# Kernel tuning notes

Hardware: AMD Instinct MI355X
Metric: run time of the kernel (lower is better)

## Reference

```python
import jax, jax.numpy as jnp
import numpy as np

T = 2048      # tokens (flattened batch*seq)
HID = 2048    # hidden_size
H = 16        # num heads
D = HID // H  # head_dim = 128
EPS = 1e-5
THETA = 1000000.0


def setup_inputs() -> dict:
    key = jax.random.key(0)
    k0, k1, k2 = jax.random.split(key, 3)
    return {
        "hidden_states": jax.random.normal(k0, (T, HID), jnp.float32),
        "positions": jnp.arange(T, dtype=jnp.int32),
        "w_qkv": jax.random.normal(k1, (HID, 3 * HID), jnp.float32) * 0.02,
        "q_norm_w": jnp.ones((HID,), jnp.float32),
        "k_norm_w": jnp.ones((HID,), jnp.float32),
        "w_o": jax.random.normal(k2, (HID, HID), jnp.float32) * 0.02,
    }


def _rmsnorm(x, w):
    # RMSNorm over the full flat q/k vector (q_size / kv_size), as in forward_native
    var = jnp.mean(jnp.square(x.astype(jnp.float32)), axis=-1, keepdims=True)
    return (x.astype(jnp.float32) * jax.lax.rsqrt(var + EPS)).astype(x.dtype) * w


def _rope(x, positions):
    # NEOX-style rotary over full head_dim. x: [T, H, D]
    half = D // 2
    inv_freq = 1.0 / (THETA ** (jnp.arange(half, dtype=jnp.float32) / half))
    ang = positions.astype(jnp.float32)[:, None] * inv_freq  # [T, half]
    cos = jnp.cos(ang)[:, None, :]  # [T, 1, half]
    sin = jnp.sin(ang)[:, None, :]
    x1, x2 = x[..., :half], x[..., half:]
    return jnp.concatenate([x1 * cos - x2 * sin, x2 * cos + x1 * sin], axis=-1)


def reference(hidden_states, positions, w_qkv, q_norm_w, k_norm_w, w_o):
    qkv = hidden_states @ w_qkv                      # [T, 3*HID]
    q, k, v = jnp.split(qkv, [HID, 2 * HID], axis=-1)
    q = _rmsnorm(q, q_norm_w)
    k = _rmsnorm(k, k_norm_w)
    q = _rope(q.reshape(T, H, D), positions)
    k = _rope(k.reshape(T, H, D), positions)
    v = v.reshape(T, H, D)
    scale = D ** -0.5
    scores = jnp.einsum('qhd,khd->hqk', q, k) * scale   # [H, T, T]
    causal = jnp.tril(jnp.ones((T, T), bool))
    scores = jnp.where(causal[None], scores, jnp.finfo(scores.dtype).min)
    probs = jax.nn.softmax(scores, axis=-1)
    attn = jnp.einsum('hqk,khd->qhd', probs, v).reshape(T, HID)
    return attn @ w_o
```

## Files before the change

kernel.cpp:

```cpp
#include <hip/hip_runtime.h>
#include <hip/hip_bf16.h>

typedef __attribute__((ext_vector_type(8))) short bf16x8;
typedef __attribute__((ext_vector_type(4))) float f32x4;

__device__ inline unsigned short f2b(float x) {
  __hip_bfloat16 b = __float2bfloat16(x);
  return *reinterpret_cast<unsigned short*>(&b);
}
__device__ inline float b2f(unsigned short u) {
  return __bfloat162float(*reinterpret_cast<const __hip_bfloat16*>(&u));
}

#define GAS(p) ((const __attribute__((address_space(1))) void*)(p))
#define LAS(p) ((__attribute__((address_space(3))) void*)(p))

__global__ __launch_bounds__(256) void cast_f32_bf16(const float* __restrict__ X,
                                                     unsigned short* __restrict__ Y, int n4) {
  int i = blockIdx.x * 256 + threadIdx.x;
  if (i < n4) {
    float4 v = reinterpret_cast<const float4*>(X)[i];
    ushort4 o;
    o.x = f2b(v.x); o.y = f2b(v.y); o.z = f2b(v.z); o.w = f2b(v.w);
    reinterpret_cast<ushort4*>(Y)[i] = o;
  }
}

__global__ __launch_bounds__(256) void tcast(const float* __restrict__ W,
                                             unsigned short* __restrict__ Wt, int K, int N) {
  __shared__ float tile[32][33];
  int n0 = blockIdx.x * 32, k0 = blockIdx.y * 32;
  int tx = threadIdx.x & 31, ty = threadIdx.x >> 5;
#pragma unroll
  for (int i = 0; i < 32; i += 8)
    tile[ty + i][tx] = W[(size_t)(k0 + ty + i) * N + n0 + tx];
  __syncthreads();
#pragma unroll
  for (int i = 0; i < 32; i += 8)
    Wt[(size_t)(n0 + ty + i) * K + k0 + tx] = f2b(tile[tx][ty + i]);
}

__global__ __launch_bounds__(256) void vtrans(const float* __restrict__ qkv,
                                              unsigned short* __restrict__ Vt) {
  __shared__ unsigned short tile[32][33];
  int c0 = blockIdx.x * 32;
  int t0 = blockIdx.y * 32;
  int tx = threadIdx.x & 31, ty = threadIdx.x >> 5;
#pragma unroll
  for (int i = 0; i < 32; i += 8)
    tile[ty + i][tx] = f2b(qkv[(size_t)(t0 + ty + i) * 6144 + 4096 + c0 + tx]);
  __syncthreads();
#pragma unroll
  for (int i = 0; i < 32; i += 8)
    Vt[(size_t)(c0 + ty + i) * 2048 + t0 + tx] = tile[tx][ty + i];
}

__global__ __launch_bounds__(256) void gemm_bt(const unsigned short* __restrict__ A,
                                               const unsigned short* __restrict__ Bt,
                                               float* __restrict__ C, int M, int N, int K) {
  __shared__ unsigned short As[128 * 32];
  __shared__ unsigned short Bs[128 * 32];
  const int tid = threadIdx.x;
  const int w = tid >> 6, l = tid & 63;
  const int lr = l & 15, lg = l >> 4;
  const int wm = (w >> 1) << 6, wn = (w & 1) << 6;
  const size_t bm = (size_t)blockIdx.y * 128, bn = (size_t)blockIdx.x * 128;

  const int srow = tid >> 2;
  const int scol = (tid & 3) << 3;
  const unsigned short* Ag = A + (bm + srow) * (size_t)K + scol;
  const unsigned short* Bg = Bt + (bn + srow) * (size_t)K + scol;
  unsigned short* Al = As + w * 512;
  unsigned short* Bl = Bs + w * 512;

  f32x4 acc[4][4] = {};

  for (int k0 = 0; k0 < K; k0 += 32) {
    __syncthreads();
    __builtin_amdgcn_global_load_lds(GAS(Ag + k0), LAS(Al), 16, 0, 0);
    __builtin_amdgcn_global_load_lds(GAS(Ag + (size_t)64 * K + k0), LAS(Al + 2048), 16, 0, 0);
    __builtin_amdgcn_global_load_lds(GAS(Bg + k0), LAS(Bl), 16, 0, 0);
    __builtin_amdgcn_global_load_lds(GAS(Bg + (size_t)64 * K + k0), LAS(Bl + 2048), 16, 0, 0);
    __syncthreads();

    bf16x8 af[4], bfr[4];
#pragma unroll
    for (int mi = 0; mi < 4; ++mi)
      af[mi] = *reinterpret_cast<const bf16x8*>(&As[(wm + mi * 16 + lr) * 32 + lg * 8]);
#pragma unroll
    for (int ni = 0; ni < 4; ++ni)
      bfr[ni] = *reinterpret_cast<const bf16x8*>(&Bs[(wn + ni * 16 + lr) * 32 + lg * 8]);
#pragma unroll
    for (int mi = 0; mi < 4; ++mi)
#pragma unroll
      for (int ni = 0; ni < 4; ++ni)
        acc[mi][ni] = __builtin_amdgcn_mfma_f32_16x16x32_bf16(af[mi], bfr[ni], acc[mi][ni], 0, 0, 0);
  }

#pragma unroll
  for (int mi = 0; mi < 4; ++mi)
#pragma unroll
    for (int ni = 0; ni < 4; ++ni)
#pragma unroll
      for (int r = 0; r < 4; ++r) {
        size_t row = bm + wm + mi * 16 + lg * 4 + r;
        size_t col = bn + wn + ni * 16 + lr;
        C[row * N + col] = acc[mi][ni][r];
      }
}

__global__ __launch_bounds__(256) void rms_rope(const float* __restrict__ qkv,
                                                const int* __restrict__ pos,
                                                const float* __restrict__ qw,
                                                const float* __restrict__ kw,
                                                unsigned short* __restrict__ qb,
                                                unsigned short* __restrict__ kb) {
  const int t = blockIdx.x;
  const float* row = qkv + (size_t)t * 6144;
  __shared__ float redq[4], redk[4];
  __shared__ float cs[64], sn[64];
  const int tid = threadIdx.x, w = tid >> 6, l = tid & 63;

  float sq = 0.f, sk = 0.f;
#pragma unroll
  for (int i = 0; i < 8; ++i) {
    float a = row[tid + i * 256]; sq += a * a;
    float b = row[2048 + tid + i * 256]; sk += b * b;
  }
#pragma unroll
  for (int m = 32; m >= 1; m >>= 1) { sq += __shfl_xor(sq, m, 64); sk += __shfl_xor(sk, m, 64); }
  if (l == 0) { redq[w] = sq; redk[w] = sk; }
  if (tid < 64) {
    float fr = exp2f(-(float)tid * 0.31143075889569016f);
    float ang = (float)pos[t] * fr;
    cs[tid] = cosf(ang);
    sn[tid] = sinf(ang);
  }
  __syncthreads();
  float rq = rsqrtf((redq[0] + redq[1] + redq[2] + redq[3]) * (1.f / 2048.f) + 1e-5f);
  float rk = rsqrtf((redk[0] + redk[1] + redk[2] + redk[3]) * (1.f / 2048.f) + 1e-5f);
  const float rqs = rq * 0.12753102543609887f;

  unsigned short* qo = qb + (size_t)t * 2048;
  unsigned short* ko = kb + (size_t)t * 2048;
#pragma unroll
  for (int pp = 0; pp < 4; ++pp) {
    int pr = tid + pp * 256;
    int h = pr >> 6, j = pr & 63;
    int b0 = h * 128 + j;
    float c = cs[j], s = sn[j];
    float x1 = row[b0] * rqs * qw[b0];
    float x2 = row[b0 + 64] * rqs * qw[b0 + 64];
    qo[b0]      = f2b(x1 * c - x2 * s);
    qo[b0 + 64] = f2b(x2 * c + x1 * s);
    float y1 = row[2048 + b0] * rk * kw[b0];
    float y2 = row[2048 + b0 + 64] * rk * kw[b0 + 64];
    ko[b0]      = f2b(y1 * c - y2 * s);
    ko[b0 + 64] = f2b(y2 * c + y1 * s);
  }
}

__device__ __forceinline__ void stage_kv(const unsigned short* __restrict__ kb_h,
                                         const unsigned short* __restrict__ vt_h,
                                         int k0, int w, int l,
                                         unsigned short* Ks, unsigned short* Vs) {
  const int r0 = l >> 4, cph = l & 15;
#pragma unroll
  for (int rb = 0; rb < 16; rb += 4) {
    int row = w * 16 + rb + r0;
    int clog = (cph & 8) | ((cph & 7) ^ (row & 7));
    const unsigned short* src = kb_h + (size_t)(k0 + row) * 2048 + clog * 8;
    __builtin_amdgcn_global_load_lds(GAS(src), LAS((char*)Ks + (w * 16 + rb) * 256), 16, 0, 0);
  }
  const int r0v = l >> 3, cpv = l & 7;
#pragma unroll
  for (int rb = 0; rb < 32; rb += 8) {
    int row = w * 32 + rb + r0v;
    int clog = cpv ^ (row & 7);
    const unsigned short* src = vt_h + (size_t)row * 2048 + k0 + clog * 8;
    __builtin_amdgcn_global_load_lds(GAS(src), LAS((char*)Vs + (w * 32 + rb) * 128), 16, 0, 0);
  }
}

template <bool MASKED>
__device__ __forceinline__ void attn_tile(int k0, int qrbase, int lr, int lg,
                                          const bf16x8 (&qf)[4],
                                          const unsigned short* __restrict__ Ks,
                                          const unsigned short* __restrict__ Vs,
                                          unsigned short* __restrict__ PsW,
                                          f32x4 (&oacc)[8], float (&mrow)[4], float (&lrow)[4]) {
  f32x4 s[4] = {};
  __builtin_amdgcn_s_setprio(1);
#pragma unroll
  for (int kc = 0; kc < 4; ++kc)
#pragma unroll
    for (int cg = 0; cg < 4; ++cg) {
      int key = cg * 16 + lr;
      int c = 4 * kc + lg;
      int cswz = (c & 8) | ((c & 7) ^ (key & 7));
      bf16x8 kf = *reinterpret_cast<const bf16x8*>(&Ks[key * 128 + cswz * 8]);
      s[cg] = __builtin_amdgcn_mfma_f32_16x16x32_bf16(qf[kc], kf, s[cg], 0, 0, 0);
    }
  __builtin_amdgcn_s_setprio(0);

#pragma unroll
  for (int r = 0; r < 4; ++r) {
    const int qr = qrbase + lg * 4 + r;
    float p0 = s[0][r], p1 = s[1][r], p2 = s[2][r], p3 = s[3][r];
    if (MASKED) {
      if (k0 + lr > qr)      p0 = -1e30f;
      if (k0 + 16 + lr > qr) p1 = -1e30f;
      if (k0 + 32 + lr > qr) p2 = -1e30f;
      if (k0 + 48 + lr > qr) p3 = -1e30f;
    }
    float mx = fmaxf(fmaxf(p0, p1), fmaxf(p2, p3));
#pragma unroll
    for (int m = 8; m >= 1; m >>= 1) mx = fmaxf(mx, __shfl_xor(mx, m, 16));
    float mnew = fmaxf(mrow[r], mx);
    float corr = exp2f(mrow[r] - mnew);
    p0 = exp2f(p0 - mnew); p1 = exp2f(p1 - mnew);
    p2 = exp2f(p2 - mnew); p3 = exp2f(p3 - mnew);
    lrow[r] = lrow[r] * corr + ((p0 + p1) + (p2 + p3));
    mrow[r] = mnew;
#pragma unroll
    for (int ni = 0; ni < 8; ++ni) oacc[ni][r] *= corr;
    const int prow = (lg * 4 + r) * 72;
    PsW[prow + lr]      = f2b(p0);
    PsW[prow + 16 + lr] = f2b(p1);
    PsW[prow + 32 + lr] = f2b(p2);
    PsW[prow + 48 + lr] = f2b(p3);
  }

  __builtin_amdgcn_s_setprio(1);
#pragma unroll
  for (int ks = 0; ks < 2; ++ks) {
    bf16x8 pf = *reinterpret_cast<const bf16x8*>(&PsW[lr * 72 + ks * 32 + lg * 8]);
#pragma unroll
    for (int ni = 0; ni < 8; ++ni) {
      int d = ni * 16 + lr;
      int c = ks * 4 + lg;
      int cswz = c ^ (d & 7);
      bf16x8 vf = *reinterpret_cast<const bf16x8*>(&Vs[d * 64 + cswz * 8]);
      oacc[ni] = __builtin_amdgcn_mfma_f32_16x16x32_bf16(pf, vf, oacc[ni], 0, 0, 0);
    }
  }
  __builtin_amdgcn_s_setprio(0);
}

__global__ __launch_bounds__(256) void attn_part(const unsigned short* __restrict__ qb,
                                                 const unsigned short* __restrict__ kb,
                                                 const unsigned short* __restrict__ vt,
                                                 unsigned short* __restrict__ Op,
                                                 float* __restrict__ ml) {
  __shared__ unsigned short Ks[64 * 128];
  __shared__ unsigned short Vs[128 * 64];
  __shared__ unsigned short Ps[4][16 * 72];
  const int qt = blockIdx.x, h = blockIdx.y, sp = blockIdx.z;
  const int q0 = qt * 64;
  const int kbeg = sp * 256;
  if (kbeg >= q0 + 64) return;
  const int tid = threadIdx.x, w = tid >> 6, l = tid & 63;
  const int lr = l & 15, lg = l >> 4;
  const int qrbase = q0 + w * 16;

  bf16x8 qf[4];
  {
    const unsigned short* qp = qb + (size_t)(qrbase + lr) * 2048 + h * 128;
#pragma unroll
    for (int kc = 0; kc < 4; ++kc)
      qf[kc] = *reinterpret_cast<const bf16x8*>(qp + kc * 32 + lg * 8);
  }
  f32x4 oacc[8] = {};
  float mrow[4], lrow[4];
#pragma unroll
  for (int r = 0; r < 4; ++r) { mrow[r] = -1e30f; lrow[r] = 0.f; }

  const unsigned short* kb_h = kb + h * 128;
  const unsigned short* vt_h = vt + (size_t)h * 128 * 2048;

  const int kstop_full = min(kbeg + 256, q0);
  for (int k0 = kbeg; k0 < kstop_full; k0 += 64) {
    __syncthreads();
    stage_kv(kb_h, vt_h, k0, w, l, Ks, Vs);
    __syncthreads();
    attn_tile<false>(k0, qrbase, lr, lg, qf, Ks, Vs, Ps[w], oacc, mrow, lrow);
  }
  if (q0 >= kbeg && q0 < kbeg + 256) {
    __syncthreads();
    stage_kv(kb_h, vt_h, q0, w, l, Ks, Vs);
    __syncthreads();
    attn_tile<true>(q0, qrbase, lr, lg, qf, Ks, Vs, Ps[w], oacc, mrow, lrow);
  }

#pragma unroll
  for (int r = 0; r < 4; ++r)
#pragma unroll
    for (int m = 8; m >= 1; m >>= 1) lrow[r] += __shfl_xor(lrow[r], m, 16);

  const int g = qt >> 2, j = qt & 3;
  const size_t u = (size_t)h * 144 + (g + 1) * (2 * g + j) + sp;
  const size_t baserow = u * 64 + w * 16;
#pragma unroll
  for (int ni = 0; ni < 8; ++ni)
#pragma unroll
    for (int r = 0; r < 4; ++r)
      Op[(baserow + lg * 4 + r) * 128 + ni * 16 + lr] = f2b(oacc[ni][r]);
  if (lr == 0) {
#pragma unroll
    for (int r = 0; r < 4; ++r) {
      size_t mi = (baserow + lg * 4 + r) * 2;
      ml[mi] = mrow[r]; ml[mi + 1] = lrow[r];
    }
  }
}

__global__ __launch_bounds__(256) void attn_combine(const unsigned short* __restrict__ Op,
                                                    const float* __restrict__ ml,
                                                    unsigned short* __restrict__ ob) {
  const int qt = blockIdx.x, h = blockIdx.y;
  const int q0 = qt * 64;
  const int g = qt >> 2, j = qt & 3;
  const int ns = g + 1;
  const size_t ubase = (size_t)h * 144 + (g + 1) * (2 * g + j);
  const int t = threadIdx.x;
  const int row = t >> 2, dp = (t & 3) * 32;

  float m_s[8], l_s[8];
  float M = -1e30f;
#pragma unroll
  for (int s = 0; s < 8; ++s) {
    if (s < ns) {
      size_t mi = ((ubase + s) * 64 + row) * 2;
      m_s[s] = ml[mi]; l_s[s] = ml[mi + 1];
    } else { m_s[s] = -1e30f; l_s[s] = 0.f; }
    M = fmaxf(M, m_s[s]);
  }
  float L = 0.f, wgt[8];
#pragma unroll
  for (int s = 0; s < 8; ++s) { wgt[s] = exp2f(m_s[s] - M); L += l_s[s] * wgt[s]; }
  float invL = 1.f / L;

  float acc[32];
#pragma unroll
  for (int jj = 0; jj < 32; ++jj) acc[jj] = 0.f;
#pragma unroll
  for (int s = 0; s < 8; ++s) {
    if (s < ns) {
      const unsigned short* op = Op + ((ubase + s) * 64 + row) * 128 + dp;
      float wg = wgt[s] * invL;
#pragma unroll
      for (int jj = 0; jj < 32; jj += 8) {
        bf16x8 v = *reinterpret_cast<const bf16x8*>(op + jj);
#pragma unroll
        for (int e = 0; e < 8; ++e) acc[jj + e] += wg * b2f((unsigned short)v[e]);
      }
    }
  }
  unsigned short* o = ob + (size_t)(q0 + row) * 2048 + h * 128 + dp;
#pragma unroll
  for (int jj = 0; jj < 32; ++jj) o[jj] = f2b(acc[jj]);
}

extern "C" void kernel_launch(void* const* d_in, const int* in_sizes, int n_in,
                              void* d_out, int out_size, void* d_ws, size_t ws_size,
                              hipStream_t stream) {
  const float* hs   = (const float*)d_in[0];
  const int*   pos  = (const int*)d_in[1];
  const float* wqkv = (const float*)d_in[2];
  const float* qnw  = (const float*)d_in[3];
  const float* knw  = (const float*)d_in[4];
  const float* wo   = (const float*)d_in[5];
  float* out = (float*)d_out;

  char* ws = (char*)d_ws;
  size_t off = 0;
  auto take = [&](size_t bytes) {
    char* p = ws + off;
    off = (off + bytes + 255) & ~(size_t)255;
    return p;
  };
  unsigned short* hidA  = (unsigned short*)take(2048ull * 2048 * 2);
  unsigned short* wqkvT = (unsigned short*)take(6144ull * 2048 * 2);
  unsigned short* woT   = (unsigned short*)take(2048ull * 2048 * 2);
  float*          qkvF  = (float*)take(2048ull * 6144 * 4);
  unsigned short* qbv   = (unsigned short*)take(2048ull * 2048 * 2);
  unsigned short* kbv   = (unsigned short*)take(2048ull * 2048 * 2);
  unsigned short* vtb   = (unsigned short*)take(2048ull * 2048 * 2);
  unsigned short* attnb = (unsigned short*)take(2048ull * 2048 * 2);
  unsigned short* Opart = (unsigned short*)qkvF;
  float*          mlb   = (float*)((char*)qkvF + 40ull * 1024 * 1024);

  cast_f32_bf16<<<4096, 256, 0, stream>>>(hs, hidA, 1048576);
  tcast<<<dim3(192, 64), 256, 0, stream>>>(wqkv, wqkvT, 2048, 6144);
  tcast<<<dim3(64, 64), 256, 0, stream>>>(wo, woT, 2048, 2048);
  gemm_bt<<<dim3(48, 16), 256, 0, stream>>>(hidA, wqkvT, qkvF, 2048, 6144, 2048);
  rms_rope<<<2048, 256, 0, stream>>>(qkvF, pos, qnw, knw, qbv, kbv);
  vtrans<<<dim3(64, 64), 256, 0, stream>>>(qkvF, vtb);
  attn_part<<<dim3(32, 16, 8), 256, 0, stream>>>(qbv, kbv, vtb, Opart, mlb);
  attn_combine<<<dim3(32, 16), 256, 0, stream>>>(Opart, mlb, attnb);
  gemm_bt<<<dim3(16, 16), 256, 0, stream>>>(attnb, woT, out, 2048, 2048, 2048);
}
```

Baseline: 374.7 us.

## Double-buffer K/V tiles in attention and widen split-K chunks to 512

The attention partial kernel now keeps two K/V shared-memory buffers. It prefetches the next 64-key tile while computing the current one, which cuts the synchronisations per tile from two to one. The key split grows from 256 to 512 keys, so there are at most four partials per query tile and the combine kernel reads fewer of them. The partial buffer now uses a simple dense [split, head, qtile] indexing. Costs are double the LDS per block, which may lower occupancy, and fewer blocks in the grid for parallelism.

```diff
diff --git a/kernel.cpp b/kernel.cpp
--- a/kernel.cpp
+++ b/kernel.cpp
@@ -252,17 +252,24 @@
                                                  const unsigned short* __restrict__ vt,
                                                  unsigned short* __restrict__ Op,
                                                  float* __restrict__ ml) {
-  __shared__ unsigned short Ks[64 * 128];
-  __shared__ unsigned short Vs[128 * 64];
+  __shared__ unsigned short Ks[2][64 * 128];
+  __shared__ unsigned short Vs[2][128 * 64];
   __shared__ unsigned short Ps[4][16 * 72];
   const int qt = blockIdx.x, h = blockIdx.y, sp = blockIdx.z;
   const int q0 = qt * 64;
-  const int kbeg = sp * 256;
+  const int kbeg = sp * 512;
   if (kbeg >= q0 + 64) return;
+  const int kend = min(kbeg + 512, q0 + 64);
+  const int nt = (kend - kbeg) >> 6;
   const int tid = threadIdx.x, w = tid >> 6, l = tid & 63;
   const int lr = l & 15, lg = l >> 4;
   const int qrbase = q0 + w * 16;
 
+  const unsigned short* kb_h = kb + h * 128;
+  const unsigned short* vt_h = vt + (size_t)h * 128 * 2048;
+
+  stage_kv(kb_h, vt_h, kbeg, w, l, Ks[0], Vs[0]);
+
   bf16x8 qf[4];
   {
     const unsigned short* qp = qb + (size_t)(qrbase + lr) * 2048 + h * 128;
@@ -275,21 +282,17 @@
 #pragma unroll
   for (int r = 0; r < 4; ++r) { mrow[r] = -1e30f; lrow[r] = 0.f; }
 
-  const unsigned short* kb_h = kb + h * 128;
-  const unsigned short* vt_h = vt + (size_t)h * 128 * 2048;
-
-  const int kstop_full = min(kbeg + 256, q0);
-  for (int k0 = kbeg; k0 < kstop_full; k0 += 64) {
+  __syncthreads();
+
+  for (int t = 0; t < nt; ++t) {
+    const int k0 = kbeg + t * 64;
+    if (t + 1 < nt)
+      stage_kv(kb_h, vt_h, k0 + 64, w, l, Ks[(t + 1) & 1], Vs[(t + 1) & 1]);
+    if (k0 == q0)
+      attn_tile<true>(k0, qrbase, lr, lg, qf, Ks[t & 1], Vs[t & 1], Ps[w], oacc, mrow, lrow);
+    else
+      attn_tile<false>(k0, qrbase, lr, lg, qf, Ks[t & 1], Vs[t & 1], Ps[w], oacc, mrow, lrow);
     __syncthreads();
-    stage_kv(kb_h, vt_h, k0, w, l, Ks, Vs);
-    __syncthreads();
-    attn_tile<false>(k0, qrbase, lr, lg, qf, Ks, Vs, Ps[w], oacc, mrow, lrow);
-  }
-  if (q0 >= kbeg && q0 < kbeg + 256) {
-    __syncthreads();
-    stage_kv(kb_h, vt_h, q0, w, l, Ks, Vs);
-    __syncthreads();
-    attn_tile<true>(q0, qrbase, lr, lg, qf, Ks, Vs, Ps[w], oacc, mrow, lrow);
   }
 
 #pragma unroll
@@ -297,18 +300,16 @@
 #pragma unroll
     for (int m = 8; m >= 1; m >>= 1) lrow[r] += __shfl_xor(lrow[r], m, 16);
 
-  const int g = qt >> 2, j = qt & 3;
-  const size_t u = (size_t)h * 144 + (g + 1) * (2 * g + j) + sp;
-  const size_t baserow = u * 64 + w * 16;
+  const size_t base = (((size_t)sp * 16 + h) * 32 + qt) * 64;
 #pragma unroll
   for (int ni = 0; ni < 8; ++ni)
 #pragma unroll
     for (int r = 0; r < 4; ++r)
-      Op[(baserow + lg * 4 + r) * 128 + ni * 16 + lr] = f2b(oacc[ni][r]);
+      Op[(base + w * 16 + lg * 4 + r) * 128 + ni * 16 + lr] = f2b(oacc[ni][r]);
   if (lr == 0) {
 #pragma unroll
     for (int r = 0; r < 4; ++r) {
-      size_t mi = (baserow + lg * 4 + r) * 2;
+      size_t mi = (base + w * 16 + lg * 4 + r) * 2;
       ml[mi] = mrow[r]; ml[mi + 1] = lrow[r];
     }
   }
@@ -319,34 +320,32 @@
                                                     unsigned short* __restrict__ ob) {
   const int qt = blockIdx.x, h = blockIdx.y;
   const int q0 = qt * 64;
-  const int g = qt >> 2, j = qt & 3;
-  const int ns = g + 1;
-  const size_t ubase = (size_t)h * 144 + (g + 1) * (2 * g + j);
+  const int ns = (qt >> 3) + 1;
   const int t = threadIdx.x;
   const int row = t >> 2, dp = (t & 3) * 32;
 
-  float m_s[8], l_s[8];
+  float m_s[4], l_s[4];
   float M = -1e30f;
 #pragma unroll
-  for (int s = 0; s < 8; ++s) {
+  for (int s = 0; s < 4; ++s) {
     if (s < ns) {
-      size_t mi = ((ubase + s) * 64 + row) * 2;
+      size_t mi = ((((size_t)s * 16 + h) * 32 + qt) * 64 + row) * 2;
       m_s[s] = ml[mi]; l_s[s] = ml[mi + 1];
     } else { m_s[s] = -1e30f; l_s[s] = 0.f; }
     M = fmaxf(M, m_s[s]);
   }
-  float L = 0.f, wgt[8];
-#pragma unroll
-  for (int s = 0; s < 8; ++s) { wgt[s] = exp2f(m_s[s] - M); L += l_s[s] * wgt[s]; }
+  float L = 0.f, wgt[4];
+#pragma unroll
+  for (int s = 0; s < 4; ++s) { wgt[s] = exp2f(m_s[s] - M); L += l_s[s] * wgt[s]; }
   float invL = 1.f / L;
 
   float acc[32];
 #pragma unroll
   for (int jj = 0; jj < 32; ++jj) acc[jj] = 0.f;
 #pragma unroll
-  for (int s = 0; s < 8; ++s) {
+  for (int s = 0; s < 4; ++s) {
     if (s < ns) {
-      const unsigned short* op = Op + ((ubase + s) * 64 + row) * 128 + dp;
+      const unsigned short* op = Op + ((((size_t)s * 16 + h) * 32 + qt) * 64 + row) * 128 + dp;
       float wg = wgt[s] * invL;
 #pragma unroll
       for (int jj = 0; jj < 32; jj += 8) {
@@ -388,7 +387,7 @@
   unsigned short* vtb   = (unsigned short*)take(2048ull * 2048 * 2);
   unsigned short* attnb = (unsigned short*)take(2048ull * 2048 * 2);
   unsigned short* Opart = (unsigned short*)qkvF;
-  float*          mlb   = (float*)((char*)qkvF + 40ull * 1024 * 1024);
+  float*          mlb   = (float*)((char*)qkvF + 32ull * 1024 * 1024);
 
   cast_f32_bf16<<<4096, 256, 0, stream>>>(hs, hidA, 1048576);
   tcast<<<dim3(192, 64), 256, 0, stream>>>(wqkv, wqkvT, 2048, 6144);
@@ -396,7 +395,7 @@
   gemm_bt<<<dim3(48, 16), 256, 0, stream>>>(hidA, wqkvT, qkvF, 2048, 6144, 2048);
   rms_rope<<<2048, 256, 0, stream>>>(qkvF, pos, qnw, knw, qbv, kbv);
   vtrans<<<dim3(64, 64), 256, 0, stream>>>(qkvF, vtb);
-  attn_part<<<dim3(32, 16, 8), 256, 0, stream>>>(qbv, kbv, vtb, Opart, mlb);
+  attn_part<<<dim3(32, 16, 4), 256, 0, stream>>>(qbv, kbv, vtb, Opart, mlb);
   attn_combine<<<dim3(32, 16), 256, 0, stream>>>(Opart, mlb, attnb);
   gemm_bt<<<dim3(16, 16), 256, 0, stream>>>(attnb, woT, out, 2048, 2048, 2048);
 }
```

Result: no change. 371.0 us (-1.0%).
